# Kernel tuning notes

Measured on AMD Instinct MI355X. Metric: run time of the kernel, lower is better.

## Reference

```python
import jax, jax.numpy as jnp
import numpy as np

ALPHA = 0.34          # Ewald splitting parameter (init kwarg alpha)
MAX_HKL = 12          # init kwarg max_hkl
TWO_PI = 2.0 * np.pi


def setup_inputs() -> dict:
    key = jax.random.key(0)
    k1, k2 = jax.random.split(key)
    N = 4096
    L = 40.0  # cubic box edge (Angstrom)
    coords = jax.random.uniform(k1, (N, 3), dtype=jnp.float32) * L
    q = jax.random.normal(k2, (N,), dtype=jnp.float32)
    q = q - jnp.mean(q)  # neutral cell (k=0 term is excluded)
    box = jnp.eye(3, dtype=jnp.float32) * L
    return {"coords": coords, "box": box, "q": q}


def _ewald_recip_energy(coords, box, q):
    """Reciprocal-space Ewald sum over |h|,|k|,|l| <= MAX_HKL (rank=0 PME fallback).

    pot_i = (4*pi/V) * sum_{k!=0} exp(-|k|^2/(4 a^2))/|k|^2 * Re[S(k) exp(-i k.r_i)]
    E     = 0.5 * sum_i q_i * pot_i
    """
    K = MAX_HKL
    vol = jnp.abs(jnp.linalg.det(box))
    recip = TWO_PI * jnp.linalg.inv(box).T  # rows = reciprocal lattice vectors (3,3)
    h = jnp.arange(-K, K + 1)
    hh, kk, ll = jnp.meshgrid(h, h, h, indexing="ij")
    hkl = jnp.stack([hh.ravel(), kk.ravel(), ll.ravel()], axis=-1).astype(jnp.float32)  # (Nk,3)
    kvecs = hkl @ recip                      # (Nk,3)
    k2 = jnp.sum(kvecs * kvecs, axis=-1)     # (Nk,)
    nonzero = k2 > 0.0                       # mask out k = 0 (static shape, jit-safe)
    k2_safe = jnp.where(nonzero, k2, 1.0)
    inv_4a2 = 1.0 / (4.0 * ALPHA * ALPHA)
    fac = jnp.where(nonzero, jnp.exp(-k2_safe * inv_4a2) / k2_safe, 0.0)  # (Nk,)
    phases = coords @ kvecs.T                # (N, Nk)
    c = jnp.cos(phases)
    s = jnp.sin(phases)
    Sre = q @ c                              # (Nk,) Re S(k)
    Sim = q @ s                              # (Nk,) Im S(k)
    pref = (4.0 * np.pi) / vol
    # Re[S(k) e^{-i k.r_i}] = Sre*cos + Sim*sin
    pot = pref * (c @ (fac * Sre) + s @ (fac * Sim))  # (N,)
    return 0.5 * jnp.sum(q * pot)


def reference(coords, box, q):
    return _ewald_recip_energy(coords, box, q)
```

## Files before the change

kernel.cpp:

```cpp
#include <hip/hip_runtime.h>
#include <math.h>

namespace {
constexpr int   KMAX   = 12;
constexpr int   NSIDE  = 2 * KMAX + 1;
constexpr int   NLINE  = 313;
constexpr int   NGROUP = NLINE * 5;
constexpr int   NKV    = NGROUP * 5;
constexpr int   NSLICE = 8;
constexpr int   SLICE_CAP = 512;
constexpr int   S2_BLOCKS = (NKV + 255) / 256;
constexpr float ALPHA_  = 0.34f;
constexpr float TWO_PI_ = 6.283185307179586f;
}

__device__ __forceinline__ void cofactors(const float* __restrict__ box,
                                          float C[3][3], float* det) {
  const float b00 = box[0], b01 = box[1], b02 = box[2];
  const float b10 = box[3], b11 = box[4], b12 = box[5];
  const float b20 = box[6], b21 = box[7], b22 = box[8];
  C[0][0] =  (b11 * b22 - b12 * b21);
  C[0][1] = -(b10 * b22 - b12 * b20);
  C[0][2] =  (b10 * b21 - b11 * b20);
  C[1][0] = -(b01 * b22 - b02 * b21);
  C[1][1] =  (b00 * b22 - b02 * b20);
  C[1][2] = -(b00 * b21 - b01 * b20);
  C[2][0] =  (b01 * b12 - b02 * b11);
  C[2][1] = -(b00 * b12 - b02 * b10);
  C[2][2] =  (b00 * b11 - b01 * b10);
  *det = b00 * C[0][0] + b01 * C[0][1] + b02 * C[0][2];
}

__device__ __forceinline__ void line_hk(int L, int* h, int* k) {
  if (L < 300)      { *h = L / 25 + 1; *k = L % 25 - 12; }
  else if (L < 312) { *h = 0;          *k = L - 299;     }
  else              { *h = 0;          *k = 0;           }
}

__global__ __launch_bounds__(256) void ewald_groups(
    const float* __restrict__ coords, const float* __restrict__ box,
    const float* __restrict__ q, int N, float* __restrict__ partial)
{
  __shared__ float4 sf[SLICE_CAP];

  float C[3][3], det;
  cofactors(box, C, &det);
  const float invdet = 1.0f / det;

  const int slice = blockIdx.y;
  const int sp    = (N + NSLICE - 1) / NSLICE;
  const int s_beg = slice * sp;
  const int s_end = min(s_beg + sp, N);

  const int lane = threadIdx.x & 63;
  const int g    = blockIdx.x * 4 + (threadIdx.x >> 6);
  const int gc   = (g < NGROUP) ? g : (NGROUP - 1);

  int h, k; line_hk(gc / 5, &h, &k);
  const float hf  = (float)h;
  const float kf  = (float)k;
  const float l0f = (float)(-KMAX + 5 * (gc % 5));

  float Sre[5] = {0.f, 0.f, 0.f, 0.f, 0.f};
  float Sim[5] = {0.f, 0.f, 0.f, 0.f, 0.f};

  for (int cb = s_beg; cb < s_end; cb += SLICE_CAP) {
    const int cnt = min(SLICE_CAP, s_end - cb);
    __syncthreads();
    for (int t = threadIdx.x; t < SLICE_CAP; t += 256) {
      float4 v = make_float4(0.f, 0.f, 0.f, 0.f);
      if (t < cnt) {
        const int gi = cb + t;
        const float x = coords[3 * gi + 0];
        const float y = coords[3 * gi + 1];
        const float z = coords[3 * gi + 2];
        v.x = (x * C[0][0] + y * C[0][1] + z * C[0][2]) * invdet;
        v.y = (x * C[1][0] + y * C[1][1] + z * C[1][2]) * invdet;
        float c = (x * C[2][0] + y * C[2][1] + z * C[2][2]) * invdet;
        v.z = c - floorf(c);
        v.w = q[gi];
      }
      sf[t] = v;
    }
    __syncthreads();

    for (int i = lane; i < SLICE_CAP; i += 64) {
      const float4 p = sf[i];
      float t = fmaf(hf, p.x, fmaf(kf, p.y, l0f * p.z));
      float tf;
      asm("v_fract_f32 %0, %1" : "=v"(tf) : "v"(t));
      float s0, c0, sr, cr;
      asm("v_sin_f32 %0, %1" : "=v"(s0) : "v"(tf));
      asm("v_cos_f32 %0, %1" : "=v"(c0) : "v"(tf));
      asm("v_sin_f32 %0, %1" : "=v"(sr) : "v"(p.z));
      asm("v_cos_f32 %0, %1" : "=v"(cr) : "v"(p.z));
      float Pre = p.w * c0, Pim = p.w * s0;
      Sre[0] += Pre; Sim[0] += Pim;
#pragma unroll
      for (int u = 1; u < 5; ++u) {
        const float nre = fmaf(Pre, cr, -(Pim * sr));
        const float nim = fmaf(Pre, sr,  (Pim * cr));
        Pre = nre; Pim = nim;
        Sre[u] += Pre; Sim[u] += Pim;
      }
    }
  }

#pragma unroll
  for (int off = 32; off > 0; off >>= 1) {
#pragma unroll
    for (int u = 0; u < 5; ++u) {
      Sre[u] += __shfl_down(Sre[u], off);
      Sim[u] += __shfl_down(Sim[u], off);
    }
  }
  if (g < NGROUP && lane == 0) {
    float* dst = partial + (size_t)(g * NSLICE + slice) * 10;
#pragma unroll
    for (int u = 0; u < 5; ++u) {
      dst[2 * u + 0] = Sre[u];
      dst[2 * u + 1] = Sim[u];
    }
  }
}

__global__ __launch_bounds__(256) void stage2(
    const float* __restrict__ partial, const float* __restrict__ box,
    float* __restrict__ bsum)
{
  __shared__ float red[256];
  const int idx = blockIdx.x * 256 + threadIdx.x;
  float e = 0.f;
  if (idx < NKV) {
    const int g = idx / 5, u = idx % 5;
    const int L = g / 5, sub = g % 5;
    int h, k; line_hk(L, &h, &k);
    const int l = -KMAX + 5 * sub + u;
    if (!(h == 0 && k == 0 && l <= 0)) {
      float re = 0.f, im = 0.f;
      for (int s = 0; s < NSLICE; ++s) {
        const float* p = partial + (size_t)(g * NSLICE + s) * 10 + 2 * u;
        re += p[0]; im += p[1];
      }
      float C[3][3], det;
      cofactors(box, C, &det);
      const float invdet = 1.0f / det;
      const float hf = (float)h, kf = (float)k, lf = (float)l;
      const float kx = (hf * C[0][0] + kf * C[1][0] + lf * C[2][0]) * invdet;
      const float ky = (hf * C[0][1] + kf * C[1][1] + lf * C[2][1]) * invdet;
      const float kz = (hf * C[0][2] + kf * C[1][2] + lf * C[2][2]) * invdet;
      const float k2 = TWO_PI_ * TWO_PI_ * (kx * kx + ky * ky + kz * kz);
      const float fac = __expf(-k2 / (4.0f * ALPHA_ * ALPHA_)) / k2;
      e = fac * fmaf(re, re, im * im);
    }
  }
  red[threadIdx.x] = e;
  __syncthreads();
  for (int s = 128; s > 0; s >>= 1) {
    if (threadIdx.x < s) red[threadIdx.x] += red[threadIdx.x + s];
    __syncthreads();
  }
  if (threadIdx.x == 0) bsum[blockIdx.x] = red[0];
}

__global__ void finalize(const float* __restrict__ bsum,
                         const float* __restrict__ box,
                         float* __restrict__ out)
{
  if (threadIdx.x == 0) {
    float acc = 0.f;
    for (int i = 0; i < S2_BLOCKS; ++i) acc += bsum[i];
    float C[3][3], det;
    cofactors(box, C, &det);
    out[0] = (4.0f * 3.14159265358979323846f / fabsf(det)) * acc;
  }
}

extern "C" void kernel_launch(void* const* d_in, const int* in_sizes, int n_in,
                              void* d_out, int out_size, void* d_ws, size_t ws_size,
                              hipStream_t stream) {
  const float* coords = (const float*)d_in[0];
  const float* box    = (const float*)d_in[1];
  const float* q      = (const float*)d_in[2];
  float* out = (float*)d_out;
  const int N = in_sizes[2];

  float* partial = (float*)d_ws;
  float* bsum    = (float*)((char*)d_ws + (512 << 10));

  const dim3 grid((NGROUP + 3) / 4, NSLICE);
  hipLaunchKernelGGL(ewald_groups, grid, dim3(256), 0, stream,
                     coords, box, q, N, partial);
  hipLaunchKernelGGL(stage2, dim3(S2_BLOCKS), dim3(256), 0, stream,
                     partial, box, bsum);
  hipLaunchKernelGGL(finalize, dim3(1), dim3(64), 0, stream, bsum, box, out);
}
```

Before: 21.54 us.

## Process full 25-point l-lines per wave with bidirectional phase recurrence

Each wavefront now owns a whole (h,k) line of 25 l-values instead of a group of 5. It starts from the l=0 phase and rotates up and down by a per-atom sin/cos of the third fractional coordinate, which is now computed once per atom in the staging loop and kept in shared memory. This cuts the number of transcendental evaluations per k-vector and the number of coords passes. In exchange, each lane holds 50 accumulator registers, the wave reduction stops at 8 partials per lane group, and stage2 must sum 64 partials per k-vector from a larger workspace (8 MB offset). Grid parallelism drops to about 79x8 blocks, which may leave the GPU underoccupied.

```diff
diff --git a/kernel.cpp b/kernel.cpp
--- a/kernel.cpp
+++ b/kernel.cpp
@@ -3,10 +3,9 @@
 
 namespace {
 constexpr int   KMAX   = 12;
-constexpr int   NSIDE  = 2 * KMAX + 1;
 constexpr int   NLINE  = 313;
-constexpr int   NGROUP = NLINE * 5;
-constexpr int   NKV    = NGROUP * 5;
+constexpr int   NL25   = 25;
+constexpr int   NKV    = NLINE * NL25;
 constexpr int   NSLICE = 8;
 constexpr int   SLICE_CAP = 512;
 constexpr int   S2_BLOCKS = (NKV + 255) / 256;
@@ -37,11 +36,12 @@
   else              { *h = 0;          *k = 0;           }
 }
 
-__global__ __launch_bounds__(256) void ewald_groups(
+__global__ __launch_bounds__(256) void ewald_lines(
     const float* __restrict__ coords, const float* __restrict__ box,
     const float* __restrict__ q, int N, float* __restrict__ partial)
 {
   __shared__ float4 sf[SLICE_CAP];
+  __shared__ float  sq[SLICE_CAP];
 
   float C[3][3], det;
   cofactors(box, C, &det);
@@ -53,22 +53,21 @@
   const int s_end = min(s_beg + sp, N);
 
   const int lane = threadIdx.x & 63;
-  const int g    = blockIdx.x * 4 + (threadIdx.x >> 6);
-  const int gc   = (g < NGROUP) ? g : (NGROUP - 1);
-
-  int h, k; line_hk(gc / 5, &h, &k);
-  const float hf  = (float)h;
-  const float kf  = (float)k;
-  const float l0f = (float)(-KMAX + 5 * (gc % 5));
-
-  float Sre[5] = {0.f, 0.f, 0.f, 0.f, 0.f};
-  float Sim[5] = {0.f, 0.f, 0.f, 0.f, 0.f};
+  const int gl   = blockIdx.x * 4 + (threadIdx.x >> 6);
+  const int line = (gl < NLINE) ? gl : (NLINE - 1);
+  int h, k; line_hk(line, &h, &k);
+  const float hf = (float)h, kf = (float)k;
+
+  float Sre[NL25], Sim[NL25];
+#pragma unroll
+  for (int u = 0; u < NL25; ++u) { Sre[u] = 0.f; Sim[u] = 0.f; }
 
   for (int cb = s_beg; cb < s_end; cb += SLICE_CAP) {
     const int cnt = min(SLICE_CAP, s_end - cb);
     __syncthreads();
     for (int t = threadIdx.x; t < SLICE_CAP; t += 256) {
-      float4 v = make_float4(0.f, 0.f, 0.f, 0.f);
+      float4 v = make_float4(0.f, 0.f, 1.f, 0.f);
+      float qq = 0.f;
       if (t < cnt) {
         const int gi = cb + t;
         const float x = coords[3 * gi + 0];
@@ -77,49 +76,59 @@
         v.x = (x * C[0][0] + y * C[0][1] + z * C[0][2]) * invdet;
         v.y = (x * C[1][0] + y * C[1][1] + z * C[1][2]) * invdet;
         float c = (x * C[2][0] + y * C[2][1] + z * C[2][2]) * invdet;
-        v.z = c - floorf(c);
-        v.w = q[gi];
+        c = c - floorf(c);
+        float cr, sr;
+        asm("v_sin_f32 %0, %1" : "=v"(sr) : "v"(c));
+        asm("v_cos_f32 %0, %1" : "=v"(cr) : "v"(c));
+        v.z = cr; v.w = sr;
+        qq = q[gi];
       }
-      sf[t] = v;
+      sf[t] = v; sq[t] = qq;
     }
     __syncthreads();
 
     for (int i = lane; i < SLICE_CAP; i += 64) {
       const float4 p = sf[i];
-      float t = fmaf(hf, p.x, fmaf(kf, p.y, l0f * p.z));
+      const float qq = sq[i];
+      float t00 = fmaf(hf, p.x, kf * p.y);
       float tf;
-      asm("v_fract_f32 %0, %1" : "=v"(tf) : "v"(t));
-      float s0, c0, sr, cr;
+      asm("v_fract_f32 %0, %1" : "=v"(tf) : "v"(t00));
+      float s0, c0;
       asm("v_sin_f32 %0, %1" : "=v"(s0) : "v"(tf));
       asm("v_cos_f32 %0, %1" : "=v"(c0) : "v"(tf));
-      asm("v_sin_f32 %0, %1" : "=v"(sr) : "v"(p.z));
-      asm("v_cos_f32 %0, %1" : "=v"(cr) : "v"(p.z));
-      float Pre = p.w * c0, Pim = p.w * s0;
-      Sre[0] += Pre; Sim[0] += Pim;
-#pragma unroll
-      for (int u = 1; u < 5; ++u) {
-        const float nre = fmaf(Pre, cr, -(Pim * sr));
-        const float nim = fmaf(Pre, sr,  (Pim * cr));
-        Pre = nre; Pim = nim;
-        Sre[u] += Pre; Sim[u] += Pim;
+      float Pur = qq * c0, Pui = qq * s0;
+      float Pdr = Pur,     Pdi = Pui;
+      Sre[12] += Pur; Sim[12] += Pui;
+      const float cr = p.z, sr = p.w;
+#pragma unroll
+      for (int u = 1; u <= 12; ++u) {
+        const float nur = fmaf(Pur, cr, -(Pui * sr));
+        const float nui = fmaf(Pur, sr,  (Pui * cr));
+        Pur = nur; Pui = nui;
+        Sre[12 + u] += Pur; Sim[12 + u] += Pui;
+        const float ndr = fmaf(Pdr, cr,  (Pdi * sr));
+        const float ndi = fmaf(Pdi, cr, -(Pdr * sr));
+        Pdr = ndr; Pdi = ndi;
+        Sre[12 - u] += Pdr; Sim[12 - u] += Pdi;
       }
     }
   }
 
 #pragma unroll
-  for (int off = 32; off > 0; off >>= 1) {
-#pragma unroll
-    for (int u = 0; u < 5; ++u) {
-      Sre[u] += __shfl_down(Sre[u], off);
-      Sim[u] += __shfl_down(Sim[u], off);
-    }
-  }
-  if (g < NGROUP && lane == 0) {
-    float* dst = partial + (size_t)(g * NSLICE + slice) * 10;
-#pragma unroll
-    for (int u = 0; u < 5; ++u) {
-      dst[2 * u + 0] = Sre[u];
-      dst[2 * u + 1] = Sim[u];
+  for (int off = 32; off >= 8; off >>= 1) {
+#pragma unroll
+    for (int u = 0; u < NL25; ++u) {
+      Sre[u] += __shfl_xor(Sre[u], off);
+      Sim[u] += __shfl_xor(Sim[u], off);
+    }
+  }
+
+  if (gl < NLINE && lane < 8) {
+    float2* dst = (float2*)partial;
+#pragma unroll
+    for (int u = 0; u < NL25; ++u) {
+      const size_t idx = ((size_t)(line * NL25 + u) * NSLICE + slice) * 8 + lane;
+      dst[idx] = make_float2(Sre[u], Sim[u]);
     }
   }
 }
@@ -132,16 +141,13 @@
   const int idx = blockIdx.x * 256 + threadIdx.x;
   float e = 0.f;
   if (idx < NKV) {
-    const int g = idx / 5, u = idx % 5;
-    const int L = g / 5, sub = g % 5;
-    int h, k; line_hk(L, &h, &k);
-    const int l = -KMAX + 5 * sub + u;
+    const int line = idx / NL25;
+    const int l    = idx % NL25 - KMAX;
+    int h, k; line_hk(line, &h, &k);
     if (!(h == 0 && k == 0 && l <= 0)) {
+      const float2* p = (const float2*)partial + (size_t)idx * (NSLICE * 8);
       float re = 0.f, im = 0.f;
-      for (int s = 0; s < NSLICE; ++s) {
-        const float* p = partial + (size_t)(g * NSLICE + s) * 10 + 2 * u;
-        re += p[0]; im += p[1];
-      }
+      for (int j = 0; j < NSLICE * 8; ++j) { re += p[j].x; im += p[j].y; }
       float C[3][3], det;
       cofactors(box, C, &det);
       const float invdet = 1.0f / det;
@@ -186,10 +192,10 @@
   const int N = in_sizes[2];
 
   float* partial = (float*)d_ws;
-  float* bsum    = (float*)((char*)d_ws + (512 << 10));
-
-  const dim3 grid((NGROUP + 3) / 4, NSLICE);
-  hipLaunchKernelGGL(ewald_groups, grid, dim3(256), 0, stream,
+  float* bsum    = (float*)((char*)d_ws + (8 << 20));
+
+  const dim3 grid((NLINE + 3) / 4, NSLICE);
+  hipLaunchKernelGGL(ewald_lines, grid, dim3(256), 0, stream,
                      coords, box, q, N, partial);
   hipLaunchKernelGGL(stage2, dim3(S2_BLOCKS), dim3(256), 0, stream,
                      partial, box, bsum);
```

After: 25.48 us. +18.3%, slower.

## Precompute per-atom z-rotation sincos, halve slices, fuse finalize via atomicAdd

Applied to the files above, without the earlier changes.

The sin/cos of the fractional z coordinate now depends only on the atom, so it is computed once when staging coordinates into shared memory rather than by every group's inner loop. This removes two transcendental ops per atom per group. Slices drop from 8 to 4, the partial buffer is laid out as float2 indexed by k-vector, and launch bounds request higher occupancy. The finalize kernel is replaced by a memset plus a per-block atomicAdd in stage2, saving a launch but making the float summation order nondeterministic.

```diff
diff --git a/kernel.cpp b/kernel.cpp
--- a/kernel.cpp
+++ b/kernel.cpp
@@ -3,11 +3,10 @@
 
 namespace {
 constexpr int   KMAX   = 12;
-constexpr int   NSIDE  = 2 * KMAX + 1;
 constexpr int   NLINE  = 313;
 constexpr int   NGROUP = NLINE * 5;
 constexpr int   NKV    = NGROUP * 5;
-constexpr int   NSLICE = 8;
+constexpr int   NSLICE = 4;
 constexpr int   SLICE_CAP = 512;
 constexpr int   S2_BLOCKS = (NKV + 255) / 256;
 constexpr float ALPHA_  = 0.34f;
@@ -37,11 +36,12 @@
   else              { *h = 0;          *k = 0;           }
 }
 
-__global__ __launch_bounds__(256) void ewald_groups(
+__global__ __launch_bounds__(256, 6) void ewald_g5(
     const float* __restrict__ coords, const float* __restrict__ box,
-    const float* __restrict__ q, int N, float* __restrict__ partial)
+    const float* __restrict__ q, int N, float2* __restrict__ partial)
 {
-  __shared__ float4 sf[SLICE_CAP];
+  __shared__ float4 sf4[SLICE_CAP];
+  __shared__ float2 sf2[SLICE_CAP];
 
   float C[3][3], det;
   cofactors(box, C, &det);
@@ -68,34 +68,40 @@
     const int cnt = min(SLICE_CAP, s_end - cb);
     __syncthreads();
     for (int t = threadIdx.x; t < SLICE_CAP; t += 256) {
-      float4 v = make_float4(0.f, 0.f, 0.f, 0.f);
+      float4 v4 = make_float4(0.f, 0.f, 1.f, 0.f);
+      float2 v2 = make_float2(0.f, 0.f);
       if (t < cnt) {
         const int gi = cb + t;
         const float x = coords[3 * gi + 0];
         const float y = coords[3 * gi + 1];
         const float z = coords[3 * gi + 2];
-        v.x = (x * C[0][0] + y * C[0][1] + z * C[0][2]) * invdet;
-        v.y = (x * C[1][0] + y * C[1][1] + z * C[1][2]) * invdet;
+        v4.x = (x * C[0][0] + y * C[0][1] + z * C[0][2]) * invdet;
+        v4.y = (x * C[1][0] + y * C[1][1] + z * C[1][2]) * invdet;
         float c = (x * C[2][0] + y * C[2][1] + z * C[2][2]) * invdet;
-        v.z = c - floorf(c);
-        v.w = q[gi];
+        c = c - floorf(c);
+        float cr, sr;
+        asm("v_sin_f32 %0, %1" : "=v"(sr) : "v"(c));
+        asm("v_cos_f32 %0, %1" : "=v"(cr) : "v"(c));
+        v4.z = cr; v4.w = sr;
+        v2.x = c;  v2.y = q[gi];
       }
-      sf[t] = v;
+      sf4[t] = v4; sf2[t] = v2;
     }
     __syncthreads();
 
+#pragma unroll 2
     for (int i = lane; i < SLICE_CAP; i += 64) {
-      const float4 p = sf[i];
-      float t = fmaf(hf, p.x, fmaf(kf, p.y, l0f * p.z));
+      const float4 p = sf4[i];
+      const float2 w = sf2[i];
+      float t0 = fmaf(hf, p.x, fmaf(kf, p.y, l0f * w.x));
       float tf;
-      asm("v_fract_f32 %0, %1" : "=v"(tf) : "v"(t));
-      float s0, c0, sr, cr;
+      asm("v_fract_f32 %0, %1" : "=v"(tf) : "v"(t0));
+      float s0, c0;
       asm("v_sin_f32 %0, %1" : "=v"(s0) : "v"(tf));
       asm("v_cos_f32 %0, %1" : "=v"(c0) : "v"(tf));
-      asm("v_sin_f32 %0, %1" : "=v"(sr) : "v"(p.z));
-      asm("v_cos_f32 %0, %1" : "=v"(cr) : "v"(p.z));
-      float Pre = p.w * c0, Pim = p.w * s0;
+      float Pre = w.y * c0, Pim = w.y * s0;
       Sre[0] += Pre; Sim[0] += Pim;
+      const float cr = p.z, sr = p.w;
 #pragma unroll
       for (int u = 1; u < 5; ++u) {
         const float nre = fmaf(Pre, cr, -(Pim * sr));
@@ -110,37 +116,36 @@
   for (int off = 32; off > 0; off >>= 1) {
 #pragma unroll
     for (int u = 0; u < 5; ++u) {
-      Sre[u] += __shfl_down(Sre[u], off);
-      Sim[u] += __shfl_down(Sim[u], off);
+      Sre[u] += __shfl_xor(Sre[u], off);
+      Sim[u] += __shfl_xor(Sim[u], off);
     }
   }
+
   if (g < NGROUP && lane == 0) {
-    float* dst = partial + (size_t)(g * NSLICE + slice) * 10;
 #pragma unroll
     for (int u = 0; u < 5; ++u) {
-      dst[2 * u + 0] = Sre[u];
-      dst[2 * u + 1] = Sim[u];
+      partial[(size_t)(g * 5 + u) * NSLICE + slice] = make_float2(Sre[u], Sim[u]);
     }
   }
 }
 
 __global__ __launch_bounds__(256) void stage2(
-    const float* __restrict__ partial, const float* __restrict__ box,
-    float* __restrict__ bsum)
+    const float2* __restrict__ partial, const float* __restrict__ box,
+    float* __restrict__ out)
 {
   __shared__ float red[256];
   const int idx = blockIdx.x * 256 + threadIdx.x;
   float e = 0.f;
   if (idx < NKV) {
     const int g = idx / 5, u = idx % 5;
-    const int L = g / 5, sub = g % 5;
-    int h, k; line_hk(L, &h, &k);
-    const int l = -KMAX + 5 * sub + u;
+    const int line = g / 5;
+    const int l = -KMAX + 5 * (g % 5) + u;
+    int h, k; line_hk(line, &h, &k);
     if (!(h == 0 && k == 0 && l <= 0)) {
       float re = 0.f, im = 0.f;
       for (int s = 0; s < NSLICE; ++s) {
-        const float* p = partial + (size_t)(g * NSLICE + s) * 10 + 2 * u;
-        re += p[0]; im += p[1];
+        const float2 p = partial[(size_t)idx * NSLICE + s];
+        re += p.x; im += p.y;
       }
       float C[3][3], det;
       cofactors(box, C, &det);
@@ -160,19 +165,11 @@
     if (threadIdx.x < s) red[threadIdx.x] += red[threadIdx.x + s];
     __syncthreads();
   }
-  if (threadIdx.x == 0) bsum[blockIdx.x] = red[0];
-}
-
-__global__ void finalize(const float* __restrict__ bsum,
-                         const float* __restrict__ box,
-                         float* __restrict__ out)
-{
   if (threadIdx.x == 0) {
-    float acc = 0.f;
-    for (int i = 0; i < S2_BLOCKS; ++i) acc += bsum[i];
     float C[3][3], det;
     cofactors(box, C, &det);
-    out[0] = (4.0f * 3.14159265358979323846f / fabsf(det)) * acc;
+    const float scale = (4.0f * 3.14159265358979323846f) / fabsf(det);
+    atomicAdd(out, scale * red[0]);
   }
 }
 
@@ -185,13 +182,12 @@
   float* out = (float*)d_out;
   const int N = in_sizes[2];
 
-  float* partial = (float*)d_ws;
-  float* bsum    = (float*)((char*)d_ws + (512 << 10));
+  float2* partial = (float2*)d_ws;
 
+  hipMemsetAsync(out, 0, sizeof(float), stream);
   const dim3 grid((NGROUP + 3) / 4, NSLICE);
-  hipLaunchKernelGGL(ewald_groups, grid, dim3(256), 0, stream,
+  hipLaunchKernelGGL(ewald_g5, grid, dim3(256), 0, stream,
                      coords, box, q, N, partial);
   hipLaunchKernelGGL(stage2, dim3(S2_BLOCKS), dim3(256), 0, stream,
-                     partial, box, bsum);
-  hipLaunchKernelGGL(finalize, dim3(1), dim3(64), 0, stream, bsum, box, out);
+                     partial, box, out);
 }
```

Result: slower. 24.15 us (+12.1%).
